# Kernel optimization log

Measured on AMD Instinct MI355X. Metric: run time of the kernel, lower is better.

Reference implementation:

```python
import jax, jax.numpy as jnp
import numpy as np

N_HEAD = 16
N_EMBD = 1024
HEAD_DIM = N_EMBD // N_HEAD  # 64
ROPE_BASE = 10000.0


def _rotary_cos_sin(T, dim, dtype=jnp.float32):
    # matches Rotary: inv_freq over even indices, cos/sin cached in bfloat16
    inv_freq = 1.0 / (ROPE_BASE ** (jnp.arange(0, dim, 2, dtype=jnp.float32) / dim))
    freqs = jnp.arange(T, dtype=jnp.float32)[:, None] * inv_freq[None, :]  # [T, dim/2]
    cos = jnp.cos(freqs).astype(jnp.bfloat16).astype(dtype)
    sin = jnp.sin(freqs).astype(jnp.bfloat16).astype(dtype)
    # shape [1, T, 1, dim/2] to broadcast over (B, T, H, d)
    return cos[None, :, None, :], sin[None, :, None, :]


def _apply_rotary(x, cos, sin):
    d = x.shape[3] // 2
    x1, x2 = x[..., :d], x[..., d:]
    y1 = x1 * cos + x2 * sin
    y2 = -x1 * sin + x2 * cos
    return jnp.concatenate([y1, y2], axis=3).astype(x.dtype)


def setup_inputs() -> dict:
    key = jax.random.key(0)
    ks = jax.random.split(key, 8)
    B, T, C = 2, 2048, N_EMBD
    scale = C ** -0.5  # realistic linear-layer init scale
    x = jax.random.normal(ks[0], (B, T, C), dtype=jnp.float32)
    Wq1 = jax.random.normal(ks[1], (C, C), dtype=jnp.float32) * scale
    Wk1 = jax.random.normal(ks[2], (C, C), dtype=jnp.float32) * scale
    Wq2 = jax.random.normal(ks[3], (C, C), dtype=jnp.float32) * scale
    Wk2 = jax.random.normal(ks[4], (C, C), dtype=jnp.float32) * scale
    Wv = jax.random.normal(ks[5], (C, C), dtype=jnp.float32) * scale
    Wout = jax.random.normal(ks[6], (C, C), dtype=jnp.float32) * scale
    return {"x": x, "Wq1": Wq1, "Wk1": Wk1, "Wq2": Wq2, "Wk2": Wk2, "Wv": Wv, "Wout": Wout}


def reference(x, Wq1, Wk1, Wq2, Wk2, Wv, Wout):
    B, T, C = x.shape
    H, D = N_HEAD, HEAD_DIM

    def proj(W):
        # torch nn.Linear(bias=False): y = x @ W.T
        return (x @ W.T).reshape(B, T, H, D)

    q1, k1 = proj(Wq1), proj(Wk1)
    q2, k2 = proj(Wq2), proj(Wk2)
    v = proj(Wv)

    cos, sin = _rotary_cos_sin(T, D, x.dtype)
    q1, k1 = _apply_rotary(q1, cos, sin), _apply_rotary(k1, cos, sin)
    q2, k2 = _apply_rotary(q2, cos, sin), _apply_rotary(k2, cos, sin)

    # two bilinear score maps, elementwise product, causal mask
    s1 = jnp.einsum('bqhd,bkhd->bhqk', q1, k1)  # [B,H,T,T]
    s2 = jnp.einsum('bqhd,bkhd->bhqk', q2, k2)
    causal = jnp.tril(jnp.ones((T, T), dtype=bool))
    pattern = jnp.where(causal[None, None], (s1 / D) * (s2 / D), 0.0)

    y = jnp.einsum('bhqk,bkhd->bqhd', pattern, v).reshape(B, T, C)
    return y @ Wout.T
```

## Files before the change

### kernel.cpp

```cpp
#include <hip/hip_runtime.h>
#include <hip/hip_bf16.h>
#include <math.h>

typedef __bf16 bf16;
typedef __bf16 bf16x8 __attribute__((ext_vector_type(8)));
typedef float  f32x4  __attribute__((ext_vector_type(4)));

#define NB    2
#define NT    2048
#define NH    16
#define ND    64
#define NC    1024
#define NBT   4096
#define NQT   32

#define AS1C(p) ((const __attribute__((address_space(1))) void*)(p))
#define AS3(p)  ((__attribute__((address_space(3))) void*)(p))

#define MFMA(a,b,c) __builtin_amdgcn_mfma_f32_16x16x32_bf16(a, b, c, 0, 0, 0)

struct WPtrs { const float* p[6]; };

__global__ void prep_kernel(const float* __restrict__ x, WPtrs w,
                            bf16* __restrict__ Xbf, bf16* __restrict__ Wcat,
                            float2* __restrict__ tbl)
{
    const int bid = blockIdx.x;
    if (bid < 4096) {
        const int i = (bid * 256 + threadIdx.x) * 4;
        float4 v = *reinterpret_cast<const float4*>(x + i);
        Xbf[i+0] = (bf16)v.x; Xbf[i+1] = (bf16)v.y;
        Xbf[i+2] = (bf16)v.z; Xbf[i+3] = (bf16)v.w;
    } else if (bid < 10240) {
        const int r   = bid - 4096;
        const int mat = r >> 10;
        const int off = ((r & 1023) * 256 + threadIdx.x) * 4;
        float4 v = *reinterpret_cast<const float4*>(w.p[mat] + off);
        bf16* d = Wcat + (size_t)mat * NC * NC + off;
        d[0] = (bf16)v.x; d[1] = (bf16)v.y; d[2] = (bf16)v.z; d[3] = (bf16)v.w;
    } else {
        const int i = (bid - 10240) * 256 + threadIdx.x;
        const int t = i >> 5, j = i & 31;
        float invf = 1.0f / powf(10000.0f, (float)j * (1.0f/32.0f));
        float fr = (float)t * invf;
        float2 cs;
        cs.x = (float)(bf16)cosf(fr);
        cs.y = (float)(bf16)sinf(fr);
        tbl[i] = cs;
    }
}

__global__ __launch_bounds__(256, 3)
void gemm_proj(const bf16* __restrict__ A, const bf16* __restrict__ Bw,
               bf16* __restrict__ qkv, const float2* __restrict__ tbl)
{
    __shared__ bf16 smem[3*8192];

    const int tid  = threadIdx.x;
    const int lane = tid & 63;
    const int w    = tid >> 6;
    const int wr   = w >> 1;
    const int wc   = w & 1;

    const int id  = blockIdx.x;
    const int xcd = id & 7;
    const int r   = id >> 3;
    const int bx  = r >> 2;
    const int by  = xcd * 4 + (r & 3);
    const int row0 = by * 128, col0 = bx * 128;

    const int lo  = lane & 15;
    const int hi  = lane >> 4;

    const int hrow = w*16 + (lane >> 2);
    const int hcol = ((lane & 3) ^ ((lane >> 3) & 3)) * 8;

    f32x4 acc[4][4] = {};

    auto stageHalf = [&](int s, int slot) {
        char* base = (char*)smem + slot * 16384;
        const int k0 = s * 32;
        #pragma unroll
        for (int i = 0; i < 2; ++i) {
            __builtin_amdgcn_global_load_lds(
                AS1C(A + (size_t)(row0 + i*64 + hrow) * NC + k0 + hcol),
                AS3(base + i*4096 + w*1024), 16, 0, 0);
            __builtin_amdgcn_global_load_lds(
                AS1C(Bw + (size_t)(col0 + i*64 + hrow) * NC + k0 + hcol),
                AS3(base + 8192 + i*4096 + w*1024), 16, 0, 0);
        }
    };

    stageHalf(0, 0);
    stageHalf(1, 1);

    const int csw = (lo >> 1) & 3;
    int slot = 0;
    for (int s = 0; s < 32; ++s) {
        if (s < 31) asm volatile("s_waitcnt vmcnt(4)" ::: "memory");
        else        asm volatile("s_waitcnt vmcnt(0)" ::: "memory");
        __builtin_amdgcn_s_barrier();
        asm volatile("" ::: "memory");
        if (s + 2 < 32) {
            int nx = slot + 2; if (nx >= 3) nx -= 3;
            stageHalf(s + 2, nx);
        }

        const char* As = (const char*)smem + slot * 16384;
        const char* Bs = As + 8192;

        bf16x8 af[4], bfr[4];
        #pragma unroll
        for (int m = 0; m < 4; ++m) {
            const int ar = wr*64 + m*16 + lo;
            af[m] = *reinterpret_cast<const bf16x8*>(As + ar*64 + ((hi ^ csw) * 16));
        }
        #pragma unroll
        for (int n = 0; n < 4; ++n) {
            const int br = wc*64 + n*16 + lo;
            bfr[n] = *reinterpret_cast<const bf16x8*>(Bs + br*64 + ((hi ^ csw) * 16));
        }
        __builtin_amdgcn_s_setprio(1);
        #pragma unroll
        for (int m = 0; m < 4; ++m)
            #pragma unroll
            for (int n = 0; n < 4; ++n)
                acc[m][n] = MFMA(af[m], bfr[n], acc[m][n]);
        __builtin_amdgcn_s_setprio(0);

        slot += 1; if (slot >= 3) slot -= 3;
    }
    __syncthreads();

    bf16* Ct = smem;
    const int p  = col0 >> 10;
    const int h0 = (col0 >> 6) & (NH-1);
    const int rb = hi * 4;

    if (p < 4) {
        const float qsc = (p == 0 || p == 2) ? 0.015625f : 1.0f;
        #pragma unroll
        for (int m = 0; m < 4; ++m)
            #pragma unroll
            for (int r2 = 0; r2 < 4; ++r2) {
                const int rl = wr*64 + m*16 + rb + r2;
                const int t  = (row0 + rl) & (NT-1);
                const unsigned key = ((unsigned)(rl >> 2) & 3) << 5;
                #pragma unroll
                for (int n = 0; n < 2; ++n) {
                    const int j = n*16 + lo;
                    float2 cs = tbl[t*32 + j];
                    float a1 = acc[m][n][r2];
                    float a2 = acc[m][n+2][r2];
                    const int c1 = wc*64 + j;
                    const int c2 = c1 + 32;
                    *(bf16*)((char*)Ct + (unsigned)(rl*256 + (((unsigned)c1*2) ^ key)))
                        = (bf16)((a1*cs.x + a2*cs.y) * qsc);
                    *(bf16*)((char*)Ct + (unsigned)(rl*256 + (((unsigned)c2*2) ^ key)))
                        = (bf16)((a2*cs.x - a1*cs.y) * qsc);
                }
            }
        __syncthreads();
        #pragma unroll
        for (int it = 0; it < 8; ++it) {
            const int chunk = it*256 + tid;
            const int rl = chunk >> 4;
            const int cc = chunk & 15;
            const unsigned key = ((unsigned)(rl >> 2) & 3) << 5;
            bf16x8 val = *reinterpret_cast<const bf16x8*>(
                (const char*)Ct + ((unsigned)rl*256 + (((unsigned)cc*16) ^ key)));
            const int rowg = row0 + rl;
            const int b = rowg >> 11;
            const int t = rowg & (NT-1);
            const int hh = h0 + (cc >> 3);
            const int d  = (cc & 7) * 8;
            *reinterpret_cast<bf16x8*>(
                qkv + ((((size_t)p*NB + b)*NH + hh)*NT + t)*ND + d) = val;
        }
    } else {
        #pragma unroll
        for (int m = 0; m < 4; ++m)
            #pragma unroll
            for (int r2 = 0; r2 < 4; ++r2) {
                const int rl = wr*64 + m*16 + rb + r2;
                #pragma unroll
                for (int n = 0; n < 4; ++n) {
                    const int c = wc*64 + n*16 + lo;
                    *(bf16*)((char*)Ct + (unsigned)(c*256 + (((unsigned)rl*2) ^ ((c&7)<<4))))
                        = (bf16)acc[m][n][r2];
                }
            }
        __syncthreads();
        const int b  = row0 >> 11;
        const int t0 = row0 & (NT-1);
        #pragma unroll
        for (int it = 0; it < 8; ++it) {
            const int chunk = it*256 + tid;
            const int c   = chunk >> 4;
            const int tcc = chunk & 15;
            bf16x8 val = *reinterpret_cast<const bf16x8*>(
                (const char*)Ct + (unsigned)(c*256 + (((unsigned)tcc*16) ^ ((c&7)<<4))));
            const int hh = h0 + (c >> 6);
            const int d  = c & 63;
            *reinterpret_cast<bf16x8*>(
                qkv + (((size_t)4*NB + b)*NH + hh)*(size_t)NT*ND
                    + (size_t)d*NT + t0 + tcc*8) = val;
        }
    }
}

__global__ __launch_bounds__(256)
void gemm_out(const bf16* __restrict__ A, const bf16* __restrict__ Bw,
              float* __restrict__ Cp)
{
    __shared__ bf16 smem[4*6144];

    const int tid  = threadIdx.x;
    const int lane = tid & 63;
    const int w    = tid >> 6;
    const int wr   = w >> 1;
    const int wc   = w & 1;
    const int row0 = blockIdx.y * 128;
    const int col0 = blockIdx.x * 64;

    const int lo  = lane & 15;
    const int hi  = lane >> 4;

    const int hrow = w*16 + (lane >> 2);
    const int hcol = ((lane & 3) ^ ((lane >> 3) & 3)) * 8;

    f32x4 acc[4][2] = {};

    auto stageHalf = [&](int s) {
        char* base = (char*)smem + (s & 3) * 12288;
        const int k0 = s * 32;
        #pragma unroll
        for (int i = 0; i < 2; ++i)
            __builtin_amdgcn_global_load_lds(
                AS1C(A + (size_t)(row0 + i*64 + hrow) * NC + k0 + hcol),
                AS3(base + i*4096 + w*1024), 16, 0, 0);
        __builtin_amdgcn_global_load_lds(
            AS1C(Bw + (size_t)(col0 + hrow) * NC + k0 + hcol),
            AS3(base + 8192 + w*1024), 16, 0, 0);
    };

    stageHalf(0);
    stageHalf(1);

    const int csw = (lo >> 1) & 3;
    for (int s = 0; s < 32; ++s) {
        if (s < 31) asm volatile("s_waitcnt vmcnt(3)" ::: "memory");
        else        asm volatile("s_waitcnt vmcnt(0)" ::: "memory");
        __builtin_amdgcn_s_barrier();
        asm volatile("" ::: "memory");
        if (s + 2 < 32) stageHalf(s + 2);

        const char* As = (const char*)smem + (s & 3) * 12288;
        const char* Bs = As + 8192;

        bf16x8 af[4], bfr[2];
        #pragma unroll
        for (int m = 0; m < 4; ++m) {
            const int ar = wr*64 + m*16 + lo;
            af[m] = *reinterpret_cast<const bf16x8*>(As + ar*64 + ((hi ^ csw) * 16));
        }
        #pragma unroll
        for (int n = 0; n < 2; ++n) {
            const int br = wc*32 + n*16 + lo;
            bfr[n] = *reinterpret_cast<const bf16x8*>(Bs + br*64 + ((hi ^ csw) * 16));
        }
        __builtin_amdgcn_s_setprio(1);
        #pragma unroll
        for (int m = 0; m < 4; ++m)
            #pragma unroll
            for (int n = 0; n < 2; ++n)
                acc[m][n] = MFMA(af[m], bfr[n], acc[m][n]);
        __builtin_amdgcn_s_setprio(0);
    }

    const int rb = hi * 4;
    #pragma unroll
    for (int m = 0; m < 4; ++m)
        #pragma unroll
        for (int n = 0; n < 2; ++n)
            #pragma unroll
            for (int r = 0; r < 4; ++r) {
                int row = row0 + wr*64 + m*16 + rb + r;
                int col = col0 + wc*32 + n*16 + lo;
                Cp[(size_t)row * NC + col] = acc[m][n][r];
            }
}

__global__ __launch_bounds__(256, 2)
void attn_kernel(const bf16* __restrict__ qkv, bf16* __restrict__ Y)
{
    __shared__ bf16 K1s[3*4096];
    __shared__ bf16 K2s[3*4096];
    __shared__ bf16 Vts[3*4096];
    __shared__ bf16 Pl [4][1024];

    const int tid  = threadIdx.x;
    const int lane = tid & 63;
    const int w    = tid >> 6;

    const int lin  = blockIdx.x;
    const int xcd  = lin & 7;
    const int slot = lin >> 3;
    const int pair = xcd * 4 + (slot >> 4);
    const int qa   = slot & 15;
    const int h    = pair >> 1;
    const int b    = pair & 1;
    const int qb   = NQT - 1 - qa;

    const size_t plane = (size_t)NB * NH * NT * ND;
    const size_t bh    = ((size_t)b * NH + h) * (size_t)NT * ND;
    const bf16* Q1 = qkv + 0*plane + bh;
    const bf16* K1 = qkv + 1*plane + bh;
    const bf16* Q2 = qkv + 2*plane + bh;
    const bf16* K2 = qkv + 3*plane + bh;
    const bf16* V  = qkv + 4*plane + bh;

    const int lo  = lane & 15;
    const int hi  = lane >> 4;
    const int hi8 = hi * 8;

    bf16x8 q1fa[2], q2fa[2], q1fb[2], q2fb[2];
    #pragma unroll
    for (int dd = 0; dd < 2; ++dd) {
        const size_t ra  = (size_t)(qa*64 + w*16 + lo) * ND + dd*32 + hi8;
        const size_t rbq = (size_t)(qb*64 + w*16 + lo) * ND + dd*32 + hi8;
        q1fa[dd] = *reinterpret_cast<const bf16x8*>(Q1 + ra);
        q2fa[dd] = *reinterpret_cast<const bf16x8*>(Q2 + ra);
        q1fb[dd] = *reinterpret_cast<const bf16x8*>(Q1 + rbq);
        q2fb[dd] = *reinterpret_cast<const bf16x8*>(Q2 + rbq);
    }

    f32x4 yacca[4] = {}, yaccb[4] = {};

    const int srow = tid >> 3;
    const int ssw  = ((tid & 7) ^ (srow & 7)) * 8;

    auto stageK = [&](int buf, int k0) {
        #pragma unroll
        for (int i = 0; i < 2; ++i) {
            const unsigned loff = (unsigned)(buf*8192 + i*4096 + w*1024);
            __builtin_amdgcn_global_load_lds(
                AS1C(K1 + (size_t)(k0 + i*32 + srow) * ND + ssw),
                AS3((char*)K1s + loff), 16, 0, 0);
            __builtin_amdgcn_global_load_lds(
                AS1C(K2 + (size_t)(k0 + i*32 + srow) * ND + ssw),
                AS3((char*)K2s + loff), 16, 0, 0);
        }
    };
    auto stageVT = [&](int buf, int k0) {
        #pragma unroll
        for (int i = 0; i < 2; ++i) {
            const int inst = w*2 + i;
            const int d    = inst*8 + (lane >> 3);
            const int sc   = ((lane & 7) ^ ((lane >> 3) & 7)) * 8;
            __builtin_amdgcn_global_load_lds(
                AS1C(V + (size_t)d * NT + k0 + sc),
                AS3((char*)Vts + (unsigned)(buf*8192 + inst*1024)), 16, 0, 0);
        }
    };

    stageK(0, 0);  stageVT(0, 0);
    stageK(1, 64); stageVT(1, 64);

    int cur = 0;
    for (int kt = 0; kt <= qb; ++kt) {
        if (kt < qb) asm volatile("s_waitcnt vmcnt(6)" ::: "memory");
        else         asm volatile("s_waitcnt vmcnt(0)" ::: "memory");
        __syncthreads();
        if (kt + 2 <= qb) {
            int nx = cur + 2; if (nx >= 3) nx -= 3;
            stageK(nx, (kt + 2) * 64);
            stageVT(nx, (kt + 2) * 64);
        }

        const bool doA = (kt <= qa);
        const bf16* K1b = K1s + cur*4096;
        const bf16* K2b = K2s + cur*4096;
        const char* Vb  = (const char*)Vts + cur*8192;

        f32x4 s1a[4] = {}, s2a[4] = {}, s1b[4] = {}, s2b[4] = {};
        __builtin_amdgcn_s_setprio(1);
        #pragma unroll
        for (int dd = 0; dd < 2; ++dd)
            #pragma unroll
            for (int sub = 0; sub < 4; ++sub) {
                const unsigned kb = (unsigned)((sub*16 + lo)*128 + (((dd*4 + hi) ^ (lo & 7)) * 16));
                bf16x8 k1f = *reinterpret_cast<const bf16x8*>((const char*)K1b + kb);
                bf16x8 k2f = *reinterpret_cast<const bf16x8*>((const char*)K2b + kb);
                s1b[sub] = MFMA(q1fb[dd], k1f, s1b[sub]);
                s2b[sub] = MFMA(q2fb[dd], k2f, s2b[sub]);
                if (doA) {
                    s1a[sub] = MFMA(q1fa[dd], k1f, s1a[sub]);
                    s2a[sub] = MFMA(q2fa[dd], k2f, s2a[sub]);
                }
            }
        __builtin_amdgcn_s_setprio(0);

        #define COMBINE(S1, S2, DIAG)                                                  \
            _Pragma("unroll")                                                          \
            for (int sub = 0; sub < 4; ++sub)                                          \
                _Pragma("unroll")                                                      \
                for (int r = 0; r < 4; ++r) {                                          \
                    const int row = hi*4 + r;                                          \
                    const int col = sub*16 + lo;                                       \
                    const unsigned byte = (unsigned)(row*128 + (((col>>3) ^ (row&7))*16) + (col&7)*2); \
                    float pv = S1[sub][r] * S2[sub][r];                                \
                    if (DIAG && col > w*16 + row) pv = 0.0f;                           \
                    *(bf16*)((char*)Pl[w] + byte) = (bf16)pv;                          \
                }

        if (kt == qb) { COMBINE(s1b, s2b, true) } else { COMBINE(s1b, s2b, false) }
        asm volatile("s_waitcnt lgkmcnt(0)" ::: "memory");
        __builtin_amdgcn_sched_barrier(0);

        bf16x8 vfr[2][4];
        __builtin_amdgcn_s_setprio(1);
        #pragma unroll
        for (int ks = 0; ks < 2; ++ks) {
            const unsigned pby = (unsigned)(lo*128 + (((ks*4 + hi) ^ (lo & 7)) * 16));
            bf16x8 pfb = *reinterpret_cast<const bf16x8*>((const char*)Pl[w] + pby);
            #pragma unroll
            for (int n = 0; n < 4; ++n) {
                const unsigned vby = (unsigned)((n*16 + lo)*128 + (((ks*4 + hi) ^ (lo & 7)) * 16));
                vfr[ks][n] = *reinterpret_cast<const bf16x8*>(Vb + vby);
                yaccb[n] = MFMA(pfb, vfr[ks][n], yaccb[n]);
            }
        }
        __builtin_amdgcn_s_setprio(0);

        if (doA) {
            asm volatile("s_waitcnt lgkmcnt(0)" ::: "memory");
            __builtin_amdgcn_sched_barrier(0);
            if (kt == qa) { COMBINE(s1a, s2a, true) } else { COMBINE(s1a, s2a, false) }
            asm volatile("s_waitcnt lgkmcnt(0)" ::: "memory");
            __builtin_amdgcn_sched_barrier(0);
            __builtin_amdgcn_s_setprio(1);
            #pragma unroll
            for (int ks = 0; ks < 2; ++ks) {
                const unsigned pby = (unsigned)(lo*128 + (((ks*4 + hi) ^ (lo & 7)) * 16));
                bf16x8 pfa = *reinterpret_cast<const bf16x8*>((const char*)Pl[w] + pby);
                #pragma unroll
                for (int n = 0; n < 4; ++n)
                    yacca[n] = MFMA(pfa, vfr[ks][n], yacca[n]);
            }
            __builtin_amdgcn_s_setprio(0);
        }
        #undef COMBINE

        cur += 1; if (cur >= 3) cur -= 3;
    }

    auto writeOut = [&](int q0, const f32x4* ya) {
        #pragma unroll
        for (int n = 0; n < 4; ++n)
            #pragma unroll
            for (int r = 0; r < 4; ++r) {
                const int row = hi*4 + r;
                const int col = n*16 + lo;
                const unsigned byte = (unsigned)(row*128 + (((col>>3) ^ (row&7))*16) + (col&7)*2);
                *(bf16*)((char*)Pl[w] + byte) = (bf16)ya[n][r];
            }
        asm volatile("s_waitcnt lgkmcnt(0)" ::: "memory");
        __builtin_amdgcn_sched_barrier(0);
        #pragma unroll
        for (int pass = 0; pass < 2; ++pass) {
            const int idx = pass*64 + lane;
            const int row = idx >> 3;
            const int cc  = idx & 7;
            bf16x8 val = *reinterpret_cast<const bf16x8*>(
                (const char*)Pl[w] + row*128 + ((cc ^ (row&7))*16));
            const int t = q0 + w*16 + row;
            const int c = h*ND + cc*8;
            *reinterpret_cast<bf16x8*>(Y + ((size_t)b*NT + t)*NC + c) = val;
        }
    };
    writeOut(qa*64, yacca);
    writeOut(qb*64, yaccb);
}

extern "C" void kernel_launch(void* const* d_in, const int* in_sizes, int n_in,
                              void* d_out, int out_size, void* d_ws, size_t ws_size,
                              hipStream_t stream)
{
    const float* x = (const float*)d_in[0];

    char* ws = (char*)d_ws;
    bf16*   Xbf   = (bf16*)ws;
    bf16*   Wcat  = (bf16*)(ws + (size_t)NBT*NC*2);
    bf16*   QKV   = (bf16*)(ws + (size_t)NBT*NC*2 + (size_t)6*NC*NC*2);
    bf16*   Ybf   = (bf16*)((char*)QKV + (size_t)5*NBT*NC*2);
    float2* tbl   = (float2*)((char*)Ybf + (size_t)NBT*NC*2);
    bf16*   Woutb = Wcat + (size_t)5*NC*NC;

    WPtrs wp;
    wp.p[0] = (const float*)d_in[1]; wp.p[1] = (const float*)d_in[2];
    wp.p[2] = (const float*)d_in[3]; wp.p[3] = (const float*)d_in[4];
    wp.p[4] = (const float*)d_in[5]; wp.p[5] = (const float*)d_in[6];

    prep_kernel<<<dim3(10496), 256, 0, stream>>>(x, wp, Xbf, Wcat, tbl);

    gemm_proj<<<dim3(1280), 256, 0, stream>>>(Xbf, Wcat, QKV, tbl);
    attn_kernel<<<dim3(512), 256, 0, stream>>>(QKV, Ybf);
    gemm_out<<<dim3(NC/64, NBT/128), 256, 0, stream>>>(Ybf, Woutb, (float*)d_out);
}
```

Measured before the change: 137.7 us.

## Software-pipeline QK score MFMAs one key tile ahead of the PV step

Restructures the attention main loop so the Q·K score MFMAs for key tile kt+1 run before the combine and P·V MFMAs of tile kt. The elementwise s1*s2 products are carried between iterations in ping-pong register arrays, and the loop is unrolled by two to alternate them. The goal is to overlap score MFMA latency with the LDS write/read and PV work of the previous tile. In exchange, each iteration now waits for all outstanding global loads (vmcnt(0)) instead of leaving one stage in flight. Register pressure also rises, and V fragments are re-read from LDS for the second query block instead of being reused.

```diff
diff --git a/kernel.cpp b/kernel.cpp
--- a/kernel.cpp
+++ b/kernel.cpp
@@ -364,96 +364,128 @@
         }
     };
 
+    #define SMFMA(SL, DA, S1A, S2A, S1B, S2B)                                          \
+        {                                                                               \
+            const char* K1b_ = (const char*)K1s + (SL)*8192;                            \
+            const char* K2b_ = (const char*)K2s + (SL)*8192;                            \
+            __builtin_amdgcn_s_setprio(1);                                              \
+            _Pragma("unroll")                                                           \
+            for (int dd = 0; dd < 2; ++dd)                                              \
+                _Pragma("unroll")                                                       \
+                for (int sub = 0; sub < 4; ++sub) {                                     \
+                    const unsigned kb = (unsigned)((sub*16 + lo)*128 +                  \
+                                        (((dd*4 + hi) ^ (lo & 7)) * 16));               \
+                    bf16x8 k1f = *reinterpret_cast<const bf16x8*>(K1b_ + kb);           \
+                    bf16x8 k2f = *reinterpret_cast<const bf16x8*>(K2b_ + kb);           \
+                    S1B[sub] = MFMA(q1fb[dd], k1f, S1B[sub]);                           \
+                    S2B[sub] = MFMA(q2fb[dd], k2f, S2B[sub]);                           \
+                    if (DA) {                                                           \
+                        S1A[sub] = MFMA(q1fa[dd], k1f, S1A[sub]);                       \
+                        S2A[sub] = MFMA(q2fa[dd], k2f, S2A[sub]);                       \
+                    }                                                                   \
+                }                                                                       \
+            __builtin_amdgcn_s_setprio(0);                                              \
+        }
+
+    #define COMBINE(P, DIAG)                                                           \
+        _Pragma("unroll")                                                              \
+        for (int sub = 0; sub < 4; ++sub)                                              \
+            _Pragma("unroll")                                                          \
+            for (int r = 0; r < 4; ++r) {                                              \
+                const int row = hi*4 + r;                                              \
+                const int col = sub*16 + lo;                                           \
+                const unsigned byte = (unsigned)(row*128 + (((col>>3) ^ (row&7))*16) + (col&7)*2); \
+                float pv = P[sub][r];                                                  \
+                if (DIAG && col > w*16 + row) pv = 0.0f;                               \
+                *(bf16*)((char*)Pl[w] + byte) = (bf16)pv;                              \
+            }
+
+    #define PVSTEP(VB, YACC)                                                           \
+        __builtin_amdgcn_s_setprio(1);                                                 \
+        _Pragma("unroll")                                                              \
+        for (int ks = 0; ks < 2; ++ks) {                                               \
+            const unsigned pby = (unsigned)(lo*128 + (((ks*4 + hi) ^ (lo & 7)) * 16)); \
+            bf16x8 pf = *reinterpret_cast<const bf16x8*>((const char*)Pl[w] + pby);    \
+            _Pragma("unroll")                                                          \
+            for (int n = 0; n < 4; ++n) {                                              \
+                const unsigned vby = (unsigned)((n*16 + lo)*128 +                      \
+                                     (((ks*4 + hi) ^ (lo & 7)) * 16));                 \
+                bf16x8 vf = *reinterpret_cast<const bf16x8*>((VB) + vby);              \
+                YACC[n] = MFMA(pf, vf, YACC[n]);                                       \
+            }                                                                          \
+        }                                                                              \
+        __builtin_amdgcn_s_setprio(0);
+
+    #define PBODY(KT, PHA, PHB, PNA, PNB)                                              \
+        {                                                                               \
+            const int  kt_   = (KT);                                                    \
+            const bool last_ = (kt_ == qb);                                             \
+            asm volatile("s_waitcnt vmcnt(0)" ::: "memory");                            \
+            __syncthreads();                                                            \
+            if (kt_ + 2 <= qb) {                                                        \
+                int nx = cur + 2; if (nx >= 3) nx -= 3;                                 \
+                stageK(nx, (kt_ + 2) * 64);                                             \
+                stageVT(nx, (kt_ + 2) * 64);                                            \
+            }                                                                           \
+            f32x4 s1a_[4] = {}, s2a_[4] = {}, s1b_[4] = {}, s2b_[4] = {};               \
+            const bool dAn_ = (kt_ + 1 <= qa);                                          \
+            int ns_ = cur + 1; if (ns_ >= 3) ns_ -= 3;                                  \
+            if (!last_) SMFMA(ns_, dAn_, s1a_, s2a_, s1b_, s2b_);                       \
+                                           \
+            const bool dA_ = (kt_ <= qa);                                               \
+            const char* Vb_ = (const char*)Vts + cur*8192;                              \
+            if (last_) { COMBINE(PHB, true) } else { COMBINE(PHB, false) }              \
+            asm volatile("s_waitcnt lgkmcnt(0)" ::: "memory");                          \
+            __builtin_amdgcn_sched_barrier(0);                                          \
+            PVSTEP(Vb_, yaccb)                                                          \
+            if (dA_) {                                                                  \
+                asm volatile("s_waitcnt lgkmcnt(0)" ::: "memory");                      \
+                __builtin_amdgcn_sched_barrier(0);                                      \
+                if (kt_ == qa) { COMBINE(PHA, true) } else { COMBINE(PHA, false) }      \
+                asm volatile("s_waitcnt lgkmcnt(0)" ::: "memory");                      \
+                __builtin_amdgcn_sched_barrier(0);                                      \
+                PVSTEP(Vb_, yacca)                                                      \
+            }                                                                           \
+                \
+            if (!last_) {                                                               \
+                _Pragma("unroll")                                                       \
+                for (int sub = 0; sub < 4; ++sub) {                                     \
+                    PNB[sub] = s1b_[sub] * s2b_[sub];                                   \
+                    if (dAn_) PNA[sub] = s1a_[sub] * s2a_[sub];                         \
+                }                                                                       \
+            }                                                                           \
+            cur += 1; if (cur >= 3) cur -= 3;                                           \
+        }
+
     stageK(0, 0);  stageVT(0, 0);
     stageK(1, 64); stageVT(1, 64);
+    asm volatile("s_waitcnt vmcnt(6)" ::: "memory");
+    __syncthreads();
+
+    f32x4 pEa[4], pEb[4], pOa[4], pOb[4];
+    {
+        f32x4 s1a_[4] = {}, s2a_[4] = {}, s1b_[4] = {}, s2b_[4] = {};
+        SMFMA(0, true, s1a_, s2a_, s1b_, s2b_);
+        #pragma unroll
+        for (int sub = 0; sub < 4; ++sub) {
+            pEb[sub] = s1b_[sub] * s2b_[sub];
+            pEa[sub] = s1a_[sub] * s2a_[sub];
+        }
+    }
 
     int cur = 0;
-    for (int kt = 0; kt <= qb; ++kt) {
-        if (kt < qb) asm volatile("s_waitcnt vmcnt(6)" ::: "memory");
-        else         asm volatile("s_waitcnt vmcnt(0)" ::: "memory");
-        __syncthreads();
-        if (kt + 2 <= qb) {
-            int nx = cur + 2; if (nx >= 3) nx -= 3;
-            stageK(nx, (kt + 2) * 64);
-            stageVT(nx, (kt + 2) * 64);
-        }
-
-        const bool doA = (kt <= qa);
-        const bf16* K1b = K1s + cur*4096;
-        const bf16* K2b = K2s + cur*4096;
-        const char* Vb  = (const char*)Vts + cur*8192;
-
-        f32x4 s1a[4] = {}, s2a[4] = {}, s1b[4] = {}, s2b[4] = {};
-        __builtin_amdgcn_s_setprio(1);
-        #pragma unroll
-        for (int dd = 0; dd < 2; ++dd)
-            #pragma unroll
-            for (int sub = 0; sub < 4; ++sub) {
-                const unsigned kb = (unsigned)((sub*16 + lo)*128 + (((dd*4 + hi) ^ (lo & 7)) * 16));
-                bf16x8 k1f = *reinterpret_cast<const bf16x8*>((const char*)K1b + kb);
-                bf16x8 k2f = *reinterpret_cast<const bf16x8*>((const char*)K2b + kb);
-                s1b[sub] = MFMA(q1fb[dd], k1f, s1b[sub]);
-                s2b[sub] = MFMA(q2fb[dd], k2f, s2b[sub]);
-                if (doA) {
-                    s1a[sub] = MFMA(q1fa[dd], k1f, s1a[sub]);
-                    s2a[sub] = MFMA(q2fa[dd], k2f, s2a[sub]);
-                }
-            }
-        __builtin_amdgcn_s_setprio(0);
-
-        #define COMBINE(S1, S2, DIAG)                                                  \
-            _Pragma("unroll")                                                          \
-            for (int sub = 0; sub < 4; ++sub)                                          \
-                _Pragma("unroll")                                                      \
-                for (int r = 0; r < 4; ++r) {                                          \
-                    const int row = hi*4 + r;                                          \
-                    const int col = sub*16 + lo;                                       \
-                    const unsigned byte = (unsigned)(row*128 + (((col>>3) ^ (row&7))*16) + (col&7)*2); \
-                    float pv = S1[sub][r] * S2[sub][r];                                \
-                    if (DIAG && col > w*16 + row) pv = 0.0f;                           \
-                    *(bf16*)((char*)Pl[w] + byte) = (bf16)pv;                          \
-                }
-
-        if (kt == qb) { COMBINE(s1b, s2b, true) } else { COMBINE(s1b, s2b, false) }
-        asm volatile("s_waitcnt lgkmcnt(0)" ::: "memory");
-        __builtin_amdgcn_sched_barrier(0);
-
-        bf16x8 vfr[2][4];
-        __builtin_amdgcn_s_setprio(1);
-        #pragma unroll
-        for (int ks = 0; ks < 2; ++ks) {
-            const unsigned pby = (unsigned)(lo*128 + (((ks*4 + hi) ^ (lo & 7)) * 16));
-            bf16x8 pfb = *reinterpret_cast<const bf16x8*>((const char*)Pl[w] + pby);
-            #pragma unroll
-            for (int n = 0; n < 4; ++n) {
-                const unsigned vby = (unsigned)((n*16 + lo)*128 + (((ks*4 + hi) ^ (lo & 7)) * 16));
-                vfr[ks][n] = *reinterpret_cast<const bf16x8*>(Vb + vby);
-                yaccb[n] = MFMA(pfb, vfr[ks][n], yaccb[n]);
-            }
-        }
-        __builtin_amdgcn_s_setprio(0);
-
-        if (doA) {
-            asm volatile("s_waitcnt lgkmcnt(0)" ::: "memory");
-            __builtin_amdgcn_sched_barrier(0);
-            if (kt == qa) { COMBINE(s1a, s2a, true) } else { COMBINE(s1a, s2a, false) }
-            asm volatile("s_waitcnt lgkmcnt(0)" ::: "memory");
-            __builtin_amdgcn_sched_barrier(0);
-            __builtin_amdgcn_s_setprio(1);
-            #pragma unroll
-            for (int ks = 0; ks < 2; ++ks) {
-                const unsigned pby = (unsigned)(lo*128 + (((ks*4 + hi) ^ (lo & 7)) * 16));
-                bf16x8 pfa = *reinterpret_cast<const bf16x8*>((const char*)Pl[w] + pby);
-                #pragma unroll
-                for (int n = 0; n < 4; ++n)
-                    yacca[n] = MFMA(pfa, vfr[ks][n], yacca[n]);
-            }
-            __builtin_amdgcn_s_setprio(0);
-        }
-        #undef COMBINE
-
-        cur += 1; if (cur >= 3) cur -= 3;
-    }
+    int kt  = 0;
+    for (;;) {
+        PBODY(kt, pEa, pEb, pOa, pOb);
+        if (++kt > qb) break;
+        PBODY(kt, pOa, pOb, pEa, pEb);
+        if (++kt > qb) break;
+    }
+
+    #undef PBODY
+    #undef PVSTEP
+    #undef COMBINE
+    #undef SMFMA
 
     auto writeOut = [&](int q0, const f32x4* ya) {
         #pragma unroll
```

Result: slower. 173.9 us (+26.3%).
